# Kernel optimization log

Hardware: AMD Instinct MI355X
Metric: run time of the kernel (lower is better)

Reference implementation:

```python
import jax, jax.numpy as jnp
import numpy as np

U, I, D = 100000, 50000, 64
N = U + I
E_G, E_U, E_I = 2400000, 1600000, 800000


def _spmm(rows, cols, vals, x, n):
    # sparse [n, m] @ dense [m, d] via gather + scale + segment-sum scatter
    return jax.ops.segment_sum(x[cols] * vals[:, None], rows, num_segments=n)


def setup_inputs() -> dict:
    key = jax.random.key(0)
    ks = jax.random.split(key, 11)
    return {
        "user_emb": jax.random.normal(ks[0], (U, D), dtype=jnp.float32),
        "item_emb": jax.random.normal(ks[1], (I, D), dtype=jnp.float32),
        "graph_rows": jax.random.randint(ks[2], (E_G,), 0, N, dtype=jnp.int32),
        "graph_cols": jax.random.randint(ks[3], (E_G,), 0, N, dtype=jnp.int32),
        "graph_vals": jax.random.uniform(ks[4], (E_G,), dtype=jnp.float32),
        "user_rows": jax.random.randint(ks[5], (E_U,), 0, U, dtype=jnp.int32),
        "user_cols": jax.random.randint(ks[6], (E_U,), 0, U, dtype=jnp.int32),
        "user_vals": jax.random.uniform(ks[7], (E_U,), dtype=jnp.float32),
        "item_rows": jax.random.randint(ks[8], (E_I,), 0, I, dtype=jnp.int32),
        "item_cols": jax.random.randint(ks[9], (E_I,), 0, I, dtype=jnp.int32),
        "item_vals": jax.random.uniform(ks[10], (E_I,), dtype=jnp.float32),
    }


def reference(user_emb, item_emb,
              graph_rows, graph_cols, graph_vals,
              user_rows, user_cols, user_vals,
              item_rows, item_cols, item_vals):
    all_emb = jnp.concatenate([user_emb, item_emb], axis=0)  # [N, D]
    all_emb1 = _spmm(graph_rows, graph_cols, graph_vals, all_emb, N)
    user_emb2 = _spmm(user_rows, user_cols, user_vals, user_emb, U)
    item_emb2 = _spmm(item_rows, item_cols, item_vals, item_emb, I)
    user_emb1, item_emb1 = all_emb1[:U], all_emb1[U:]
    return (user_emb1, item_emb1, user_emb2, item_emb2)
```

## Files before the change

### kernel.cpp

```cpp
#include <hip/hip_runtime.h>

#define DDIM 64
constexpr int U_CNT = 100000;
constexpr int I_CNT = 50000;
constexpr int N_CNT = U_CNT + I_CNT;
constexpr int NB    = N_CNT + U_CNT + I_CNT;

constexpr int BIN_ROWS_LOG = 8;
constexpr int BIN_ROWS = 1 << BIN_ROWS_LOG;
constexpr int BINS = (NB + BIN_ROWS - 1) / BIN_ROWS;
constexpr int BINS_PAD = 1536;
constexpr int SORT_EDGES = 4096;
constexpr int HIST_EDGES = 32768;
constexpr int CAP = 4672;

constexpr int SB_LOG = 12;
constexpr int NSB = (NB + (1 << SB_LOG) - 1) >> SB_LOG;
constexpr int NSB_PAD = 128;

__device__ __forceinline__ int wave_incl_scan(int v, int lane) {
#pragma unroll
    for (int off = 1; off < 64; off <<= 1) {
        int t = __shfl_up(v, off, 64);
        if (lane >= off) v += t;
    }
    return v;
}

__device__ __forceinline__ unsigned short f2bf_rne(float f) {
    unsigned u = __float_as_uint(f);
    unsigned r = (u + 0x7FFFu + ((u >> 16) & 1u)) >> 16;
    return (unsigned short)r;
}

__global__ __launch_bounds__(256) void convert_emb(const float* __restrict__ ue,
                                                   const float* __restrict__ ie,
                                                   unsigned short* __restrict__ emb16) {
    int g = blockIdx.x * 256 + threadIdx.x;
    constexpr int UG = U_CNT * (DDIM / 4);
    constexpr int TG = N_CNT * (DDIM / 4);
    if (g >= TG) return;
    float4 v = (g < UG) ? ((const float4*)ue)[g] : ((const float4*)ie)[g - UG];
    ushort4 o;
    o.x = f2bf_rne(v.x); o.y = f2bf_rne(v.y); o.z = f2bf_rne(v.z); o.w = f2bf_rne(v.w);
    ((ushort4*)emb16)[g] = o;
}

__global__ __launch_bounds__(1024) void hist_pre(const int* __restrict__ gr,
                                                 const int* __restrict__ ur,
                                                 const int* __restrict__ ir,
                                                 int EG, int EU, int EI,
                                                 int* __restrict__ cnt) {
    __shared__ int h[BINS_PAD];
    for (int i = threadIdx.x; i < BINS_PAD; i += 1024) h[i] = 0;
    __syncthreads();
    int base = blockIdx.x * HIST_EDGES;
    int Et = EG + EU + EI;
    for (int j = 0; j < HIST_EDGES / 1024; ++j) {
        int e = base + j * 1024 + threadIdx.x;
        if (e < Et) {
            int b;
            if (e < EG)           b = gr[e];
            else if (e < EG + EU) b = N_CNT + ur[e - EG];
            else                  b = N_CNT + U_CNT + ir[e - EG - EU];
            atomicAdd(&h[b >> BIN_ROWS_LOG], 1);
        }
    }
    __syncthreads();
    for (int i = threadIdx.x; i < BINS; i += 1024) {
        int v = h[i];
        if (v) atomicAdd(&cnt[i], v);
    }
}

__global__ __launch_bounds__(1024) void scan_bins(const int* __restrict__ cnt,
                                                  int* __restrict__ bin_base,
                                                  int* __restrict__ bin_cursor,
                                                  int* __restrict__ sb_base,
                                                  int* __restrict__ sb_cursor,
                                                  int E_total) {
    __shared__ int wsum[16], woff[16];
    int tid = threadIdx.x, lane = tid & 63, wid = tid >> 6;
    int i0 = 2 * tid, i1 = 2 * tid + 1;
    int c0 = (i0 < BINS) ? cnt[i0] : 0;
    int c1 = (i1 < BINS) ? cnt[i1] : 0;
    int v = c0 + c1;
    int incl = wave_incl_scan(v, lane);
    if (lane == 63) wsum[wid] = incl;
    __syncthreads();
    if (wid == 0 && lane < 16) {
        int s = wsum[lane], si = s;
#pragma unroll
        for (int off = 1; off < 16; off <<= 1) {
            int t = __shfl_up(si, off, 64);
            if (lane >= off) si += t;
        }
        woff[lane] = si - s;
    }
    __syncthreads();
    int e = incl - v + woff[wid];
    if (i0 < BINS) { bin_base[i0] = e;      bin_cursor[i0] = e; }
    if (i1 < BINS) { bin_base[i1] = e + c0; bin_cursor[i1] = e + c0; }
    if (tid == 0) bin_base[BINS] = E_total;
    if (sb_base) {
        __syncthreads();
        if (tid <= NSB) {
            int idx = tid << (SB_LOG - BIN_ROWS_LOG);
            int vv = (idx >= BINS) ? E_total : bin_base[idx];
            sb_base[tid] = vv;
            if (tid < NSB) sb_cursor[tid] = vv;
        }
    }
}

__global__ __launch_bounds__(512) void sbsort(const int* __restrict__ rows,
                                              const int* __restrict__ cols,
                                              const float* __restrict__ vals, int E,
                                              int bucket_base, int gidx_base,
                                              int* __restrict__ sb_cursor,
                                              uint2* __restrict__ poolA) {
    __shared__ uint2 sorted[SORT_EDGES];
    __shared__ unsigned char ssb[SORT_EDGES];
    __shared__ int hist[NSB_PAD];
    __shared__ int lscan[NSB_PAD];
    __shared__ int lcur[NSB_PAD];
    __shared__ int wsum2[2];

    int tid = threadIdx.x, lane = tid & 63, wid = tid >> 6;
    for (int i = tid; i < NSB_PAD; i += 512) { hist[i] = 0; lcur[i] = 0; }
    __syncthreads();

    int start = blockIdx.x * SORT_EDGES;
    int base_e = start + tid * 8;
    int myb[8]; unsigned mylo[8]; float myv[8];
#pragma unroll
    for (int j = 0; j < 8; j += 4) {
        int e = base_e + j;
        if (e + 3 < E) {
            int4   r4 = *(const int4*)(rows + e);
            int4   c4 = *(const int4*)(cols + e);
            float4 v4 = *(const float4*)(vals + e);
            int rr[4] = {r4.x, r4.y, r4.z, r4.w};
            int cc[4] = {c4.x, c4.y, c4.z, c4.w};
            float vv[4] = {v4.x, v4.y, v4.z, v4.w};
#pragma unroll
            for (int q = 0; q < 4; ++q) {
                int bucket = bucket_base + rr[q];
                int sb = bucket >> SB_LOG;
                myb[j + q] = sb;
                mylo[j + q] = ((unsigned)(bucket & 4095) << 18) |
                              (unsigned)(gidx_base + cc[q]);
                myv[j + q] = vv[q];
                atomicAdd(&hist[sb], 1);
            }
        } else {
#pragma unroll
            for (int q = 0; q < 4; ++q) {
                int ee = e + q;
                if (ee < E) {
                    int bucket = bucket_base + rows[ee];
                    int sb = bucket >> SB_LOG;
                    myb[j + q] = sb;
                    mylo[j + q] = ((unsigned)(bucket & 4095) << 18) |
                                  (unsigned)(gidx_base + cols[ee]);
                    myv[j + q] = vals[ee];
                    atomicAdd(&hist[sb], 1);
                } else myb[j + q] = -1;
            }
        }
    }
    __syncthreads();

    int v = 0, incl = 0;
    if (tid < NSB_PAD) {
        v = hist[tid];
        incl = wave_incl_scan(v, lane);
        if (lane == 63) wsum2[wid] = incl;
    }
    __syncthreads();
    if (tid < NSB_PAD) {
        int st = incl - v + (wid ? wsum2[0] : 0);
        lscan[tid] = st;
        if (tid < NSB && v) hist[tid] = atomicAdd(&sb_cursor[tid], v);
    }
    __syncthreads();

#pragma unroll
    for (int j = 0; j < 8; ++j) {
        if (myb[j] >= 0) {
            int p = lscan[myb[j]] + atomicAdd(&lcur[myb[j]], 1);
            sorted[p] = make_uint2(mylo[j], __float_as_uint(myv[j]));
            ssb[p] = (unsigned char)myb[j];
        }
    }
    __syncthreads();

    int cntE = min(SORT_EDGES, E - start);
    for (int pos = tid; pos < cntE; pos += 512) {
        int b = ssb[pos];
        poolA[hist[b] + (pos - lscan[b])] = sorted[pos];
    }
}

__global__ __launch_bounds__(512) void binsort2(const uint2* __restrict__ poolA,
                                                const int* __restrict__ sb_base, int Et,
                                                int* __restrict__ bin_cursor,
                                                uint2* __restrict__ poolB) {
    __shared__ uint2 sorted[SORT_EDGES];
    __shared__ unsigned short sbin[SORT_EDGES];
    __shared__ int hist[BINS_PAD];
    __shared__ int lscan[BINS_PAD];
    __shared__ int lcur[BINS_PAD];
    __shared__ int wsum[8], woff[8];
    __shared__ int ssbb[NSB + 1];

    int tid = threadIdx.x, lane = tid & 63, wid = tid >> 6;
    for (int i = tid; i < BINS_PAD; i += 512) { hist[i] = 0; lcur[i] = 0; }
    if (tid <= NSB) ssbb[tid] = sb_base[tid];
    __syncthreads();

    int start = blockIdx.x * SORT_EDGES;
    int base_e = start + tid * 8;
    int sb;
    {
        int lo2 = 0, hi2 = NSB - 1;
        while (lo2 < hi2) {
            int mid = (lo2 + hi2 + 1) >> 1;
            if (ssbb[mid] <= base_e) lo2 = mid; else hi2 = mid - 1;
        }
        sb = lo2;
    }

    int myb[8]; uint2 myp[8];
#pragma unroll
    for (int j = 0; j < 8; j += 2) {
        int e = base_e + j;
        uint2 p0, p1;
        bool v1 = (e + 1 < Et), v0 = (e < Et);
        if (v1) {
            uint4 q = *(const uint4*)(poolA + e);
            p0 = make_uint2(q.x, q.y); p1 = make_uint2(q.z, q.w);
        } else if (v0) {
            p0 = poolA[e];
        }
        if (v0) {
            while (sb < NSB - 1 && e >= ssbb[sb + 1]) ++sb;
            int b = (sb << (SB_LOG - BIN_ROWS_LOG)) + (int)(p0.x >> 26);
            myb[j] = b; myp[j] = p0;
            atomicAdd(&hist[b], 1);
        } else myb[j] = -1;
        if (v1) {
            int e1 = e + 1;
            while (sb < NSB - 1 && e1 >= ssbb[sb + 1]) ++sb;
            int b = (sb << (SB_LOG - BIN_ROWS_LOG)) + (int)(p1.x >> 26);
            myb[j + 1] = b; myp[j + 1] = p1;
            atomicAdd(&hist[b], 1);
        } else myb[j + 1] = -1;
    }
    __syncthreads();

    int s0 = 3 * tid, s1 = s0 + 1, s2 = s0 + 2;
    int h0 = hist[s0], h1 = hist[s1], h2 = hist[s2];
    int v = h0 + h1 + h2;
    int incl = wave_incl_scan(v, lane);
    if (lane == 63) wsum[wid] = incl;
    __syncthreads();
    if (wid == 0 && lane < 8) {
        int s = wsum[lane], si = s;
#pragma unroll
        for (int off = 1; off < 8; off <<= 1) {
            int t = __shfl_up(si, off, 64);
            if (lane >= off) si += t;
        }
        woff[lane] = si - s;
    }
    __syncthreads();
    int e0 = incl - v + woff[wid];
    lscan[s0] = e0; lscan[s1] = e0 + h0; lscan[s2] = e0 + h0 + h1;
    if (s0 < BINS && h0) hist[s0] = atomicAdd(&bin_cursor[s0], h0);
    if (s1 < BINS && h1) hist[s1] = atomicAdd(&bin_cursor[s1], h1);
    if (s2 < BINS && h2) hist[s2] = atomicAdd(&bin_cursor[s2], h2);
    __syncthreads();

#pragma unroll
    for (int j = 0; j < 8; ++j) {
        if (myb[j] >= 0) {
            int p = lscan[myb[j]] + atomicAdd(&lcur[myb[j]], 1);
            sorted[p] = myp[j];
            sbin[p] = (unsigned short)myb[j];
        }
    }
    __syncthreads();

    int cntE = min(SORT_EDGES, Et - start);
    for (int pos = tid; pos < cntE; pos += 512) {
        int b = sbin[pos];
        poolB[hist[b] + (pos - lscan[b])] = sorted[pos];
    }
}

__global__ __launch_bounds__(512) void binsort(const int* __restrict__ rows,
                                               const int* __restrict__ cols,
                                               const float* __restrict__ vals, int E,
                                               int bucket_base, int gidx_base,
                                               int* __restrict__ bin_cursor,
                                               uint2* __restrict__ pool) {
    __shared__ uint2 sorted[SORT_EDGES];
    __shared__ unsigned short sbin[SORT_EDGES];
    __shared__ int hist[BINS_PAD];
    __shared__ int lscan[BINS_PAD];
    __shared__ int lcur[BINS_PAD];
    __shared__ int wsum[8], woff[8];

    int tid = threadIdx.x, lane = tid & 63, wid = tid >> 6;
    for (int i = tid; i < BINS_PAD; i += 512) { hist[i] = 0; lcur[i] = 0; }
    __syncthreads();

    int start = blockIdx.x * SORT_EDGES;
    int base_e = start + tid * 8;
    int myb[8]; unsigned mylo[8]; float myv[8];
#pragma unroll
    for (int j = 0; j < 8; j += 4) {
        int e = base_e + j;
        if (e + 3 < E) {
            int4   r4 = *(const int4*)(rows + e);
            int4   c4 = *(const int4*)(cols + e);
            float4 v4 = *(const float4*)(vals + e);
            int rr[4] = {r4.x, r4.y, r4.z, r4.w};
            int cc[4] = {c4.x, c4.y, c4.z, c4.w};
            float vv[4] = {v4.x, v4.y, v4.z, v4.w};
#pragma unroll
            for (int q = 0; q < 4; ++q) {
                int bucket = bucket_base + rr[q];
                myb[j + q] = bucket >> BIN_ROWS_LOG;
                mylo[j + q] = ((unsigned)(bucket & (BIN_ROWS - 1)) << 18) |
                              (unsigned)(gidx_base + cc[q]);
                myv[j + q] = vv[q];
                atomicAdd(&hist[myb[j + q]], 1);
            }
        } else {
#pragma unroll
            for (int q = 0; q < 4; ++q) {
                int ee = e + q;
                if (ee < E) {
                    int bucket = bucket_base + rows[ee];
                    myb[j + q] = bucket >> BIN_ROWS_LOG;
                    mylo[j + q] = ((unsigned)(bucket & (BIN_ROWS - 1)) << 18) |
                                  (unsigned)(gidx_base + cols[ee]);
                    myv[j + q] = vals[ee];
                    atomicAdd(&hist[myb[j + q]], 1);
                } else myb[j + q] = -1;
            }
        }
    }
    __syncthreads();

    int s0 = 3 * tid, s1 = s0 + 1, s2 = s0 + 2;
    int h0 = hist[s0], h1 = hist[s1], h2 = hist[s2];
    int v = h0 + h1 + h2;
    int incl = wave_incl_scan(v, lane);
    if (lane == 63) wsum[wid] = incl;
    __syncthreads();
    if (wid == 0 && lane < 8) {
        int s = wsum[lane], si = s;
#pragma unroll
        for (int off = 1; off < 8; off <<= 1) {
            int t = __shfl_up(si, off, 64);
            if (lane >= off) si += t;
        }
        woff[lane] = si - s;
    }
    __syncthreads();
    int e0 = incl - v + woff[wid];
    lscan[s0] = e0; lscan[s1] = e0 + h0; lscan[s2] = e0 + h0 + h1;
    if (s0 < BINS && h0) hist[s0] = atomicAdd(&bin_cursor[s0], h0);
    if (s1 < BINS && h1) hist[s1] = atomicAdd(&bin_cursor[s1], h1);
    if (s2 < BINS && h2) hist[s2] = atomicAdd(&bin_cursor[s2], h2);
    __syncthreads();

#pragma unroll
    for (int j = 0; j < 8; ++j) {
        if (myb[j] >= 0) {
            int p = lscan[myb[j]] + atomicAdd(&lcur[myb[j]], 1);
            sorted[p] = make_uint2(mylo[j], __float_as_uint(myv[j]));
            sbin[p] = (unsigned short)myb[j];
        }
    }
    __syncthreads();

    int cntE = min(SORT_EDGES, E - start);
    for (int pos = tid; pos < cntE; pos += 512) {
        int b = sbin[pos];
        pool[hist[b] + (pos - lscan[b])] = sorted[pos];
    }
}

template <bool BF16>
__global__ __launch_bounds__(512, 8) void refine_accum(const int* __restrict__ bin_base,
                                                       const uint2* __restrict__ pool,
                                                       const unsigned short* __restrict__ emb16,
                                                       const float* __restrict__ ue,
                                                       const float* __restrict__ ie,
                                                       float* __restrict__ out) {
    __shared__ uint2 sorted[CAP];
    __shared__ int rhist[BIN_ROWS];
    __shared__ int rstart[BIN_ROWS];
    __shared__ int rcur[BIN_ROWS];
    __shared__ int wsum[4];
    int tid = threadIdx.x, lane = tid & 63, wid = tid >> 6;
    int b = blockIdx.x;
    int s = bin_base[b], e = bin_base[b + 1];
    int cnt = min(e - s, CAP);

    if (tid < BIN_ROWS) rhist[tid] = 0;
    __syncthreads();

    const unsigned* px = (const unsigned*)pool;
    for (int i = tid; i < cnt; i += 512)
        atomicAdd(&rhist[(px[2 * (size_t)(s + i)] >> 18) & 255u], 1);
    __syncthreads();

    int v = 0, incl = 0;
    if (tid < BIN_ROWS) {
        v = rhist[tid];
        incl = wave_incl_scan(v, lane);
        if (lane == 63) wsum[wid] = incl;
    }
    __syncthreads();
    if (tid < BIN_ROWS) {
        int off = 0;
#pragma unroll
        for (int w = 0; w < 4; ++w)
            if (w < wid) off += wsum[w];
        int st = incl - v + off;
        rstart[tid] = st; rcur[tid] = st;
    }
    __syncthreads();

    for (int i = tid; i < cnt; i += 512) {
        uint2 p = pool[s + i];
        int pos = atomicAdd(&rcur[(p.x >> 18) & 255u], 1);
        sorted[pos] = p;
    }
    __syncthreads();

    long long rowbase = (long long)b * BIN_ROWS;
    auto gather = [&](unsigned gi) -> float {
        if (BF16) return __uint_as_float((unsigned)emb16[(gi << 6) + lane] << 16);
        return (gi < (unsigned)U_CNT) ? ue[((size_t)gi << 6) + lane]
                                      : ie[(((size_t)gi - U_CNT) << 6) + lane];
    };
    for (int r = wid; r < BIN_ROWS; r += 8) {
        long long row = rowbase + r;
        if (row >= NB) break;
        int k = rstart[r], ke = k + rhist[r];
        float acc0 = 0.f, acc1 = 0.f;
        for (; k + 8 <= ke; k += 8) {
            uint2 p0 = sorted[k],     p1 = sorted[k + 1], p2 = sorted[k + 2], p3 = sorted[k + 3];
            uint2 p4 = sorted[k + 4], p5 = sorted[k + 5], p6 = sorted[k + 6], p7 = sorted[k + 7];
            float x0 = gather(p0.x & 0x3FFFFu);
            float x1 = gather(p1.x & 0x3FFFFu);
            float x2 = gather(p2.x & 0x3FFFFu);
            float x3 = gather(p3.x & 0x3FFFFu);
            float x4 = gather(p4.x & 0x3FFFFu);
            float x5 = gather(p5.x & 0x3FFFFu);
            float x6 = gather(p6.x & 0x3FFFFu);
            float x7 = gather(p7.x & 0x3FFFFu);
            acc0 += __uint_as_float(p0.y) * x0;
            acc1 += __uint_as_float(p1.y) * x1;
            acc0 += __uint_as_float(p2.y) * x2;
            acc1 += __uint_as_float(p3.y) * x3;
            acc0 += __uint_as_float(p4.y) * x4;
            acc1 += __uint_as_float(p5.y) * x5;
            acc0 += __uint_as_float(p6.y) * x6;
            acc1 += __uint_as_float(p7.y) * x7;
        }
        for (; k + 4 <= ke; k += 4) {
            uint2 p0 = sorted[k], p1 = sorted[k + 1], p2 = sorted[k + 2], p3 = sorted[k + 3];
            float x0 = gather(p0.x & 0x3FFFFu);
            float x1 = gather(p1.x & 0x3FFFFu);
            float x2 = gather(p2.x & 0x3FFFFu);
            float x3 = gather(p3.x & 0x3FFFFu);
            acc0 += __uint_as_float(p0.y) * x0;
            acc1 += __uint_as_float(p1.y) * x1;
            acc0 += __uint_as_float(p2.y) * x2;
            acc1 += __uint_as_float(p3.y) * x3;
        }
        for (; k < ke; ++k) {
            uint2 p = sorted[k];
            acc0 += __uint_as_float(p.y) * gather(p.x & 0x3FFFFu);
        }
        out[(size_t)row * DDIM + lane] = acc0 + acc1;
    }
}

__global__ void spmm_graph_kernel(const int* __restrict__ rows, const int* __restrict__ cols,
                                  const float* __restrict__ vals,
                                  const float* __restrict__ user_emb,
                                  const float* __restrict__ item_emb,
                                  float* __restrict__ out, int E) {
    long long idx = (long long)blockIdx.x * blockDim.x + threadIdx.x;
    int e = (int)(idx >> 6), d = (int)(idx & 63);
    if (e >= E) return;
    int r = rows[e], c = cols[e];
    float v = vals[e];
    float x = (c < U_CNT) ? user_emb[(long long)c * DDIM + d]
                          : item_emb[(long long)(c - U_CNT) * DDIM + d];
    atomicAdd(&out[(long long)r * DDIM + d], v * x);
}

__global__ void spmm_plain_kernel(const int* __restrict__ rows, const int* __restrict__ cols,
                                  const float* __restrict__ vals,
                                  const float* __restrict__ emb,
                                  float* __restrict__ out, int E) {
    long long idx = (long long)blockIdx.x * blockDim.x + threadIdx.x;
    int e = (int)(idx >> 6), d = (int)(idx & 63);
    if (e >= E) return;
    int r = rows[e], c = cols[e];
    atomicAdd(&out[(long long)r * DDIM + d], vals[e] * emb[(long long)c * DDIM + d]);
}

extern "C" void kernel_launch(void* const* d_in, const int* in_sizes, int n_in,
                              void* d_out, int out_size, void* d_ws, size_t ws_size,
                              hipStream_t stream) {
    const float* user_emb = (const float*)d_in[0];
    const float* item_emb = (const float*)d_in[1];
    const int*   g_rows   = (const int*)d_in[2];
    const int*   g_cols   = (const int*)d_in[3];
    const float* g_vals   = (const float*)d_in[4];
    const int*   u_rows   = (const int*)d_in[5];
    const int*   u_cols   = (const int*)d_in[6];
    const float* u_vals   = (const float*)d_in[7];
    const int*   i_rows   = (const int*)d_in[8];
    const int*   i_cols   = (const int*)d_in[9];
    const float* i_vals   = (const float*)d_in[10];
    float* out = (float*)d_out;

    const int EG = in_sizes[2];
    const int EU = in_sizes[5];
    const int EI = in_sizes[8];
    const int Et = EG + EU + EI;

    const size_t emb_bytes = (size_t)N_CNT * DDIM * sizeof(unsigned short);

    size_t t_off_bb   = (size_t)BINS_PAD * sizeof(int);
    size_t t_off_bc   = t_off_bb + (size_t)(BINS + 1) * sizeof(int);
    size_t t_off_sbb  = t_off_bc + (size_t)BINS * sizeof(int);
    size_t t_off_sbc  = t_off_sbb + (size_t)(NSB + 1) * sizeof(int);
    size_t t_off_pa   = (t_off_sbc + (size_t)NSB * sizeof(int) + 15) & ~(size_t)15;
    size_t t_off_pb   = t_off_pa + (size_t)Et * sizeof(uint2);
    size_t needed_2p  = t_off_pb + (size_t)Et * sizeof(uint2);
    bool pa_fits_emb  = (size_t)Et * sizeof(uint2) >= emb_bytes;

    size_t o_off_base   = (size_t)BINS_PAD * sizeof(int);
    size_t o_off_cursor = o_off_base + (size_t)(BINS + 1) * sizeof(int);
    size_t o_off_pool   = (o_off_cursor + (size_t)BINS * sizeof(int) + 15) & ~(size_t)15;
    size_t o_off_emb    = o_off_pool + (size_t)Et * sizeof(uint2);
    size_t needed_min   = o_off_emb;
    size_t needed_full  = o_off_emb + emb_bytes;

    if (ws_size >= needed_2p && pa_fits_emb) {
        int*   cnt        = (int*)d_ws;
        int*   bin_base   = (int*)((char*)d_ws + t_off_bb);
        int*   bin_cursor = (int*)((char*)d_ws + t_off_bc);
        int*   sb_base    = (int*)((char*)d_ws + t_off_sbb);
        int*   sb_cursor  = (int*)((char*)d_ws + t_off_sbc);
        uint2* poolA      = (uint2*)((char*)d_ws + t_off_pa);
        uint2* poolB      = (uint2*)((char*)d_ws + t_off_pb);
        unsigned short* emb16 = (unsigned short*)poolA;

        hipMemsetAsync(cnt, 0, (size_t)BINS_PAD * sizeof(int), stream);

        unsigned hblocks = (unsigned)((Et + HIST_EDGES - 1) / HIST_EDGES);
        hist_pre<<<hblocks, 1024, 0, stream>>>(g_rows, u_rows, i_rows, EG, EU, EI, cnt);
        scan_bins<<<1, 1024, 0, stream>>>(cnt, bin_base, bin_cursor, sb_base, sb_cursor, Et);

        unsigned gb = (unsigned)((EG + SORT_EDGES - 1) / SORT_EDGES);
        unsigned ub = (unsigned)((EU + SORT_EDGES - 1) / SORT_EDGES);
        unsigned ib = (unsigned)((EI + SORT_EDGES - 1) / SORT_EDGES);
        sbsort<<<gb, 512, 0, stream>>>(g_rows, g_cols, g_vals, EG, 0,             0,     sb_cursor, poolA);
        sbsort<<<ub, 512, 0, stream>>>(u_rows, u_cols, u_vals, EU, N_CNT,         0,     sb_cursor, poolA);
        sbsort<<<ib, 512, 0, stream>>>(i_rows, i_cols, i_vals, EI, N_CNT + U_CNT, U_CNT, sb_cursor, poolA);

        unsigned b2 = (unsigned)((Et + SORT_EDGES - 1) / SORT_EDGES);
        binsort2<<<b2, 512, 0, stream>>>(poolA, sb_base, Et, bin_cursor, poolB);

        unsigned cgrid = (unsigned)((N_CNT * (DDIM / 4) + 255) / 256);
        convert_emb<<<cgrid, 256, 0, stream>>>(user_emb, item_emb, emb16);

        refine_accum<true><<<BINS, 512, 0, stream>>>(bin_base, poolB, emb16,
                                                     user_emb, item_emb, out);
    } else if (ws_size >= needed_min) {
        int*   cnt        = (int*)d_ws;
        int*   bin_base   = (int*)((char*)d_ws + o_off_base);
        int*   bin_cursor = (int*)((char*)d_ws + o_off_cursor);
        uint2* pool       = (uint2*)((char*)d_ws + o_off_pool);
        unsigned short* emb16 = (unsigned short*)((char*)d_ws + o_off_emb);
        bool use_bf16 = (ws_size >= needed_full);

        hipMemsetAsync(cnt, 0, (size_t)BINS_PAD * sizeof(int), stream);

        if (use_bf16) {
            unsigned cgrid = (unsigned)((N_CNT * (DDIM / 4) + 255) / 256);
            convert_emb<<<cgrid, 256, 0, stream>>>(user_emb, item_emb, emb16);
        }

        unsigned hblocks = (unsigned)((Et + HIST_EDGES - 1) / HIST_EDGES);
        hist_pre<<<hblocks, 1024, 0, stream>>>(g_rows, u_rows, i_rows, EG, EU, EI, cnt);
        scan_bins<<<1, 1024, 0, stream>>>(cnt, bin_base, bin_cursor, nullptr, nullptr, Et);

        unsigned gb = (unsigned)((EG + SORT_EDGES - 1) / SORT_EDGES);
        unsigned ub = (unsigned)((EU + SORT_EDGES - 1) / SORT_EDGES);
        unsigned ib = (unsigned)((EI + SORT_EDGES - 1) / SORT_EDGES);
        binsort<<<gb, 512, 0, stream>>>(g_rows, g_cols, g_vals, EG, 0,             0,     bin_cursor, pool);
        binsort<<<ub, 512, 0, stream>>>(u_rows, u_cols, u_vals, EU, N_CNT,         0,     bin_cursor, pool);
        binsort<<<ib, 512, 0, stream>>>(i_rows, i_cols, i_vals, EI, N_CNT + U_CNT, U_CNT, bin_cursor, pool);

        if (use_bf16)
            refine_accum<true><<<BINS, 512, 0, stream>>>(bin_base, pool, emb16,
                                                         user_emb, item_emb, out);
        else
            refine_accum<false><<<BINS, 512, 0, stream>>>(bin_base, pool, (const unsigned short*)nullptr,
                                                          user_emb, item_emb, out);
    } else {
        hipMemsetAsync(d_out, 0, (size_t)out_size * sizeof(float), stream);
        const int block = 256;
        {
            long long t = (long long)EG * DDIM;
            spmm_graph_kernel<<<(unsigned)((t + block - 1) / block), block, 0, stream>>>(
                g_rows, g_cols, g_vals, user_emb, item_emb, out, EG);
        }
        {
            long long t = (long long)EU * DDIM;
            spmm_plain_kernel<<<(unsigned)((t + block - 1) / block), block, 0, stream>>>(
                u_rows, u_cols, u_vals, user_emb, out + (size_t)N_CNT * DDIM, EU);
        }
        {
            long long t = (long long)EI * DDIM;
            spmm_plain_kernel<<<(unsigned)((t + block - 1) / block), block, 0, stream>>>(
                i_rows, i_cols, i_vals, item_emb, out + (size_t)(N_CNT + U_CNT) * DDIM, EI);
        }
    }
}
```

Baseline: 376.5 us.

## Fuse bf16 conversion into histogram, merge sort launches, window binsort2, nontemporal traffic

The bf16 embedding conversion now runs inside the histogram kernel, using a separate workspace region when it fits. The three per-matrix superbucket sort launches become one kernel. binsort2 keeps a 48-bin local window and scatters edges outside it directly with global atomics, replacing a 1536-entry shared scan. Loads and stores of the sort pools and output become nontemporal, and refine_accum caches its pool entries in registers so it no longer reads them twice. The aim is fewer launches and less memory traffic, at the cost of extra global atomics for out-of-window edges and a larger workspace requirement.

```diff
diff --git a/kernel.cpp b/kernel.cpp
--- a/kernel.cpp
+++ b/kernel.cpp
@@ -11,12 +11,17 @@
 constexpr int BINS = (NB + BIN_ROWS - 1) / BIN_ROWS;
 constexpr int BINS_PAD = 1536;
 constexpr int SORT_EDGES = 4096;
-constexpr int HIST_EDGES = 32768;
+constexpr int HIST_EDGES = 16384;
 constexpr int CAP = 4672;
+constexpr int NSLOT = 10;
 
 constexpr int SB_LOG = 12;
 constexpr int NSB = (NB + (1 << SB_LOG) - 1) >> SB_LOG;
 constexpr int NSB_PAD = 128;
+constexpr int BWIN = 48;
+
+typedef unsigned u32x2 __attribute__((ext_vector_type(2)));
+typedef unsigned u32x4 __attribute__((ext_vector_type(4)));
 
 __device__ __forceinline__ int wave_incl_scan(int v, int lane) {
 #pragma unroll
@@ -46,14 +51,30 @@
     ((ushort4*)emb16)[g] = o;
 }
 
-__global__ __launch_bounds__(1024) void hist_pre(const int* __restrict__ gr,
-                                                 const int* __restrict__ ur,
-                                                 const int* __restrict__ ir,
-                                                 int EG, int EU, int EI,
-                                                 int* __restrict__ cnt) {
+__global__ __launch_bounds__(1024) void hist_conv(const int* __restrict__ gr,
+                                                  const int* __restrict__ ur,
+                                                  const int* __restrict__ ir,
+                                                  int EG, int EU, int EI,
+                                                  int* __restrict__ cnt,
+                                                  const float* __restrict__ ue,
+                                                  const float* __restrict__ ie,
+                                                  unsigned short* __restrict__ emb16) {
     __shared__ int h[BINS_PAD];
     for (int i = threadIdx.x; i < BINS_PAD; i += 1024) h[i] = 0;
-    __syncthreads();
+
+    if (emb16) {
+        constexpr int UG = U_CNT * (DDIM / 4);
+        constexpr int TG = N_CNT * (DDIM / 4);
+        int stride = (int)gridDim.x * 1024;
+        for (int g = blockIdx.x * 1024 + threadIdx.x; g < TG; g += stride) {
+            float4 v = (g < UG) ? ((const float4*)ue)[g] : ((const float4*)ie)[g - UG];
+            ushort4 o;
+            o.x = f2bf_rne(v.x); o.y = f2bf_rne(v.y); o.z = f2bf_rne(v.z); o.w = f2bf_rne(v.w);
+            ((ushort4*)emb16)[g] = o;
+        }
+    }
+    __syncthreads();
+
     int base = blockIdx.x * HIST_EDGES;
     int Et = EG + EU + EI;
     for (int j = 0; j < HIST_EDGES / 1024; ++j) {
@@ -113,12 +134,12 @@
     }
 }
 
-__global__ __launch_bounds__(512) void sbsort(const int* __restrict__ rows,
-                                              const int* __restrict__ cols,
-                                              const float* __restrict__ vals, int E,
-                                              int bucket_base, int gidx_base,
-                                              int* __restrict__ sb_cursor,
-                                              uint2* __restrict__ poolA) {
+__global__ __launch_bounds__(512, 6) void sbsort_all(
+        const int* __restrict__ gr, const int* __restrict__ gc, const float* __restrict__ gv,
+        const int* __restrict__ ur, const int* __restrict__ uc, const float* __restrict__ uv,
+        const int* __restrict__ ir, const int* __restrict__ ic, const float* __restrict__ iv,
+        int EG, int EU, int EI,
+        int* __restrict__ sb_cursor, uint2* __restrict__ poolA) {
     __shared__ uint2 sorted[SORT_EDGES];
     __shared__ unsigned char ssb[SORT_EDGES];
     __shared__ int hist[NSB_PAD];
@@ -130,26 +151,33 @@
     for (int i = tid; i < NSB_PAD; i += 512) { hist[i] = 0; lcur[i] = 0; }
     __syncthreads();
 
+    const int Et = EG + EU + EI;
     int start = blockIdx.x * SORT_EDGES;
     int base_e = start + tid * 8;
     int myb[8]; unsigned mylo[8]; float myv[8];
+
 #pragma unroll
     for (int j = 0; j < 8; j += 4) {
         int e = base_e + j;
-        if (e + 3 < E) {
-            int4   r4 = *(const int4*)(rows + e);
-            int4   c4 = *(const int4*)(cols + e);
-            float4 v4 = *(const float4*)(vals + e);
+        int sg0 = (e < EG) ? 0 : (e < EG + EU ? 1 : 2);
+        int sg3 = (e + 3 < EG) ? 0 : (e + 3 < EG + EU ? 1 : 2);
+        if (e + 3 < Et && sg0 == sg3) {
+            const int* R; const int* Cc; const float* V; int boff, goff, loc;
+            if (sg0 == 0)      { R = gr; Cc = gc; V = gv; boff = 0;             goff = 0;     loc = e; }
+            else if (sg0 == 1) { R = ur; Cc = uc; V = uv; boff = N_CNT;         goff = 0;     loc = e - EG; }
+            else               { R = ir; Cc = ic; V = iv; boff = N_CNT + U_CNT; goff = U_CNT; loc = e - EG - EU; }
+            int4   r4 = *(const int4*)(R + loc);
+            int4   c4 = *(const int4*)(Cc + loc);
+            float4 v4 = *(const float4*)(V + loc);
             int rr[4] = {r4.x, r4.y, r4.z, r4.w};
             int cc[4] = {c4.x, c4.y, c4.z, c4.w};
             float vv[4] = {v4.x, v4.y, v4.z, v4.w};
 #pragma unroll
             for (int q = 0; q < 4; ++q) {
-                int bucket = bucket_base + rr[q];
+                int bucket = boff + rr[q];
                 int sb = bucket >> SB_LOG;
                 myb[j + q] = sb;
-                mylo[j + q] = ((unsigned)(bucket & 4095) << 18) |
-                              (unsigned)(gidx_base + cc[q]);
+                mylo[j + q] = ((unsigned)(bucket & 4095) << 18) | (unsigned)(goff + cc[q]);
                 myv[j + q] = vv[q];
                 atomicAdd(&hist[sb], 1);
             }
@@ -157,13 +185,16 @@
 #pragma unroll
             for (int q = 0; q < 4; ++q) {
                 int ee = e + q;
-                if (ee < E) {
-                    int bucket = bucket_base + rows[ee];
+                if (ee < Et) {
+                    int r, c; float vl; int boff, goff;
+                    if (ee < EG)           { r = gr[ee]; c = gc[ee]; vl = gv[ee]; boff = 0; goff = 0; }
+                    else if (ee < EG + EU) { int k = ee - EG;      r = ur[k]; c = uc[k]; vl = uv[k]; boff = N_CNT;         goff = 0; }
+                    else                   { int k = ee - EG - EU; r = ir[k]; c = ic[k]; vl = iv[k]; boff = N_CNT + U_CNT; goff = U_CNT; }
+                    int bucket = boff + r;
                     int sb = bucket >> SB_LOG;
                     myb[j + q] = sb;
-                    mylo[j + q] = ((unsigned)(bucket & 4095) << 18) |
-                                  (unsigned)(gidx_base + cols[ee]);
-                    myv[j + q] = vals[ee];
+                    mylo[j + q] = ((unsigned)(bucket & 4095) << 18) | (unsigned)(goff + c);
+                    myv[j + q] = vl;
                     atomicAdd(&hist[sb], 1);
                 } else myb[j + q] = -1;
             }
@@ -195,27 +226,29 @@
     }
     __syncthreads();
 
-    int cntE = min(SORT_EDGES, E - start);
+    int cntE = min(SORT_EDGES, Et - start);
     for (int pos = tid; pos < cntE; pos += 512) {
         int b = ssb[pos];
-        poolA[hist[b] + (pos - lscan[b])] = sorted[pos];
-    }
-}
-
-__global__ __launch_bounds__(512) void binsort2(const uint2* __restrict__ poolA,
-                                                const int* __restrict__ sb_base, int Et,
-                                                int* __restrict__ bin_cursor,
-                                                uint2* __restrict__ poolB) {
+        uint2 t = sorted[pos];
+        u32x2 q; q.x = t.x; q.y = t.y;
+        __builtin_nontemporal_store(q, (u32x2*)&poolA[hist[b] + (pos - lscan[b])]);
+    }
+}
+
+__global__ __launch_bounds__(512, 6) void binsort2(const uint2* __restrict__ poolA,
+                                                   const int* __restrict__ sb_base, int Et,
+                                                   int* __restrict__ bin_cursor,
+                                                   uint2* __restrict__ poolB) {
     __shared__ uint2 sorted[SORT_EDGES];
-    __shared__ unsigned short sbin[SORT_EDGES];
-    __shared__ int hist[BINS_PAD];
-    __shared__ int lscan[BINS_PAD];
-    __shared__ int lcur[BINS_PAD];
-    __shared__ int wsum[8], woff[8];
+    __shared__ unsigned char sbin[SORT_EDGES];
+    __shared__ int hist[BWIN];
+    __shared__ int lscan[BWIN];
+    __shared__ int lcur[BWIN];
     __shared__ int ssbb[NSB + 1];
-
-    int tid = threadIdx.x, lane = tid & 63, wid = tid >> 6;
-    for (int i = tid; i < BINS_PAD; i += 512) { hist[i] = 0; lcur[i] = 0; }
+    __shared__ int W0s, nloc;
+
+    int tid = threadIdx.x, lane = tid & 63;
+    if (tid < BWIN) { hist[tid] = 0; }
     if (tid <= NSB) ssbb[tid] = sb_base[tid];
     __syncthreads();
 
@@ -230,6 +263,9 @@
         }
         sb = lo2;
     }
+    if (tid == 0) W0s = sb << (SB_LOG - BIN_ROWS_LOG);
+    __syncthreads();
+    int W0 = W0s;
 
     int myb[8]; uint2 myp[8];
 #pragma unroll
@@ -238,64 +274,69 @@
         uint2 p0, p1;
         bool v1 = (e + 1 < Et), v0 = (e < Et);
         if (v1) {
-            uint4 q = *(const uint4*)(poolA + e);
-            p0 = make_uint2(q.x, q.y); p1 = make_uint2(q.z, q.w);
+            u32x4 q = __builtin_nontemporal_load((const u32x4*)(poolA + e));
+            p0.x = q.x; p0.y = q.y; p1.x = q.z; p1.y = q.w;
         } else if (v0) {
-            p0 = poolA[e];
+            u32x2 q = __builtin_nontemporal_load((const u32x2*)(poolA + e));
+            p0.x = q.x; p0.y = q.y;
         }
         if (v0) {
             while (sb < NSB - 1 && e >= ssbb[sb + 1]) ++sb;
             int b = (sb << (SB_LOG - BIN_ROWS_LOG)) + (int)(p0.x >> 26);
-            myb[j] = b; myp[j] = p0;
-            atomicAdd(&hist[b], 1);
+            int slot = b - W0;
+            if ((unsigned)slot < (unsigned)BWIN) {
+                myb[j] = slot; myp[j] = p0;
+                atomicAdd(&hist[slot], 1);
+            } else {
+                int gp = atomicAdd(&bin_cursor[b], 1);
+                poolB[gp] = p0;
+                myb[j] = -1;
+            }
         } else myb[j] = -1;
         if (v1) {
             int e1 = e + 1;
             while (sb < NSB - 1 && e1 >= ssbb[sb + 1]) ++sb;
             int b = (sb << (SB_LOG - BIN_ROWS_LOG)) + (int)(p1.x >> 26);
-            myb[j + 1] = b; myp[j + 1] = p1;
-            atomicAdd(&hist[b], 1);
+            int slot = b - W0;
+            if ((unsigned)slot < (unsigned)BWIN) {
+                myb[j + 1] = slot; myp[j + 1] = p1;
+                atomicAdd(&hist[slot], 1);
+            } else {
+                int gp = atomicAdd(&bin_cursor[b], 1);
+                poolB[gp] = p1;
+                myb[j + 1] = -1;
+            }
         } else myb[j + 1] = -1;
     }
     __syncthreads();
 
-    int s0 = 3 * tid, s1 = s0 + 1, s2 = s0 + 2;
-    int h0 = hist[s0], h1 = hist[s1], h2 = hist[s2];
-    int v = h0 + h1 + h2;
-    int incl = wave_incl_scan(v, lane);
-    if (lane == 63) wsum[wid] = incl;
-    __syncthreads();
-    if (wid == 0 && lane < 8) {
-        int s = wsum[lane], si = s;
-#pragma unroll
-        for (int off = 1; off < 8; off <<= 1) {
-            int t = __shfl_up(si, off, 64);
-            if (lane >= off) si += t;
-        }
-        woff[lane] = si - s;
-    }
-    __syncthreads();
-    int e0 = incl - v + woff[wid];
-    lscan[s0] = e0; lscan[s1] = e0 + h0; lscan[s2] = e0 + h0 + h1;
-    if (s0 < BINS && h0) hist[s0] = atomicAdd(&bin_cursor[s0], h0);
-    if (s1 < BINS && h1) hist[s1] = atomicAdd(&bin_cursor[s1], h1);
-    if (s2 < BINS && h2) hist[s2] = atomicAdd(&bin_cursor[s2], h2);
+    if (tid < 64) {
+        int vv = (tid < BWIN) ? hist[tid] : 0;
+        int incl = wave_incl_scan(vv, lane);
+        if (tid < BWIN) { lscan[tid] = incl - vv; lcur[tid] = incl - vv; }
+        if (tid == BWIN - 1) nloc = incl;
+    }
+    __syncthreads();
+    if (tid < BWIN && hist[tid] > 0)
+        hist[tid] = atomicAdd(&bin_cursor[W0 + tid], hist[tid]);
     __syncthreads();
 
 #pragma unroll
     for (int j = 0; j < 8; ++j) {
         if (myb[j] >= 0) {
-            int p = lscan[myb[j]] + atomicAdd(&lcur[myb[j]], 1);
+            int p = atomicAdd(&lcur[myb[j]], 1);
             sorted[p] = myp[j];
-            sbin[p] = (unsigned short)myb[j];
-        }
-    }
-    __syncthreads();
-
-    int cntE = min(SORT_EDGES, Et - start);
-    for (int pos = tid; pos < cntE; pos += 512) {
-        int b = sbin[pos];
-        poolB[hist[b] + (pos - lscan[b])] = sorted[pos];
+            sbin[p] = (unsigned char)myb[j];
+        }
+    }
+    __syncthreads();
+
+    int tot = nloc;
+    for (int pos = tid; pos < tot; pos += 512) {
+        int sl = sbin[pos];
+        uint2 t = sorted[pos];
+        u32x2 q; q.x = t.x; q.y = t.y;
+        __builtin_nontemporal_store(q, (u32x2*)&poolB[hist[sl] + (pos - lscan[sl])]);
     }
 }
 
@@ -415,9 +456,17 @@
     if (tid < BIN_ROWS) rhist[tid] = 0;
     __syncthreads();
 
-    const unsigned* px = (const unsigned*)pool;
-    for (int i = tid; i < cnt; i += 512)
-        atomicAdd(&rhist[(px[2 * (size_t)(s + i)] >> 18) & 255u], 1);
+    uint2 my[NSLOT];
+    const u32x2* poolv = (const u32x2*)(pool + s);
+#pragma unroll
+    for (int j = 0; j < NSLOT; ++j) {
+        int idx = tid + j * 512;
+        if (idx < cnt) {
+            u32x2 q = __builtin_nontemporal_load(poolv + idx);
+            my[j].x = q.x; my[j].y = q.y;
+            atomicAdd(&rhist[(q.x >> 18) & 255u], 1);
+        }
+    }
     __syncthreads();
 
     int v = 0, incl = 0;
@@ -437,10 +486,13 @@
     }
     __syncthreads();
 
-    for (int i = tid; i < cnt; i += 512) {
-        uint2 p = pool[s + i];
-        int pos = atomicAdd(&rcur[(p.x >> 18) & 255u], 1);
-        sorted[pos] = p;
+#pragma unroll
+    for (int j = 0; j < NSLOT; ++j) {
+        int idx = tid + j * 512;
+        if (idx < cnt) {
+            int pos = atomicAdd(&rcur[(my[j].x >> 18) & 255u], 1);
+            sorted[pos] = my[j];
+        }
     }
     __syncthreads();
 
@@ -490,7 +542,7 @@
             uint2 p = sorted[k];
             acc0 += __uint_as_float(p.y) * gather(p.x & 0x3FFFFu);
         }
-        out[(size_t)row * DDIM + lane] = acc0 + acc1;
+        __builtin_nontemporal_store(acc0 + acc1, &out[(size_t)row * DDIM + lane]);
     }
 }
 
@@ -550,6 +602,8 @@
     size_t t_off_pa   = (t_off_sbc + (size_t)NSB * sizeof(int) + 15) & ~(size_t)15;
     size_t t_off_pb   = t_off_pa + (size_t)Et * sizeof(uint2);
     size_t needed_2p  = t_off_pb + (size_t)Et * sizeof(uint2);
+    size_t t_off_emb  = (needed_2p + 15) & ~(size_t)15;
+    size_t needed_na  = t_off_emb + emb_bytes;
     bool pa_fits_emb  = (size_t)Et * sizeof(uint2) >= emb_bytes;
 
     size_t o_off_base   = (size_t)BINS_PAD * sizeof(int);
@@ -560,6 +614,7 @@
     size_t needed_full  = o_off_emb + emb_bytes;
 
     if (ws_size >= needed_2p && pa_fits_emb) {
+        bool noalias = (ws_size >= needed_na);
         int*   cnt        = (int*)d_ws;
         int*   bin_base   = (int*)((char*)d_ws + t_off_bb);
         int*   bin_cursor = (int*)((char*)d_ws + t_off_bc);
@@ -567,26 +622,28 @@
         int*   sb_cursor  = (int*)((char*)d_ws + t_off_sbc);
         uint2* poolA      = (uint2*)((char*)d_ws + t_off_pa);
         uint2* poolB      = (uint2*)((char*)d_ws + t_off_pb);
-        unsigned short* emb16 = (unsigned short*)poolA;
+        unsigned short* emb16 = noalias ? (unsigned short*)((char*)d_ws + t_off_emb)
+                                        : (unsigned short*)poolA;
 
         hipMemsetAsync(cnt, 0, (size_t)BINS_PAD * sizeof(int), stream);
 
         unsigned hblocks = (unsigned)((Et + HIST_EDGES - 1) / HIST_EDGES);
-        hist_pre<<<hblocks, 1024, 0, stream>>>(g_rows, u_rows, i_rows, EG, EU, EI, cnt);
+        hist_conv<<<hblocks, 1024, 0, stream>>>(g_rows, u_rows, i_rows, EG, EU, EI, cnt,
+                                                user_emb, item_emb,
+                                                noalias ? emb16 : (unsigned short*)nullptr);
         scan_bins<<<1, 1024, 0, stream>>>(cnt, bin_base, bin_cursor, sb_base, sb_cursor, Et);
 
-        unsigned gb = (unsigned)((EG + SORT_EDGES - 1) / SORT_EDGES);
-        unsigned ub = (unsigned)((EU + SORT_EDGES - 1) / SORT_EDGES);
-        unsigned ib = (unsigned)((EI + SORT_EDGES - 1) / SORT_EDGES);
-        sbsort<<<gb, 512, 0, stream>>>(g_rows, g_cols, g_vals, EG, 0,             0,     sb_cursor, poolA);
-        sbsort<<<ub, 512, 0, stream>>>(u_rows, u_cols, u_vals, EU, N_CNT,         0,     sb_cursor, poolA);
-        sbsort<<<ib, 512, 0, stream>>>(i_rows, i_cols, i_vals, EI, N_CNT + U_CNT, U_CNT, sb_cursor, poolA);
-
-        unsigned b2 = (unsigned)((Et + SORT_EDGES - 1) / SORT_EDGES);
-        binsort2<<<b2, 512, 0, stream>>>(poolA, sb_base, Et, bin_cursor, poolB);
-
-        unsigned cgrid = (unsigned)((N_CNT * (DDIM / 4) + 255) / 256);
-        convert_emb<<<cgrid, 256, 0, stream>>>(user_emb, item_emb, emb16);
+        unsigned nb2 = (unsigned)((Et + SORT_EDGES - 1) / SORT_EDGES);
+        sbsort_all<<<nb2, 512, 0, stream>>>(g_rows, g_cols, g_vals,
+                                            u_rows, u_cols, u_vals,
+                                            i_rows, i_cols, i_vals,
+                                            EG, EU, EI, sb_cursor, poolA);
+        binsort2<<<nb2, 512, 0, stream>>>(poolA, sb_base, Et, bin_cursor, poolB);
+
+        if (!noalias) {
+            unsigned cgrid = (unsigned)((N_CNT * (DDIM / 4) + 255) / 256);
+            convert_emb<<<cgrid, 256, 0, stream>>>(user_emb, item_emb, emb16);
+        }
 
         refine_accum<true><<<BINS, 512, 0, stream>>>(bin_base, poolB, emb16,
                                                      user_emb, item_emb, out);
@@ -600,13 +657,10 @@
 
         hipMemsetAsync(cnt, 0, (size_t)BINS_PAD * sizeof(int), stream);
 
-        if (use_bf16) {
-            unsigned cgrid = (unsigned)((N_CNT * (DDIM / 4) + 255) / 256);
-            convert_emb<<<cgrid, 256, 0, stream>>>(user_emb, item_emb, emb16);
-        }
-
         unsigned hblocks = (unsigned)((Et + HIST_EDGES - 1) / HIST_EDGES);
-        hist_pre<<<hblocks, 1024, 0, stream>>>(g_rows, u_rows, i_rows, EG, EU, EI, cnt);
+        hist_conv<<<hblocks, 1024, 0, stream>>>(g_rows, u_rows, i_rows, EG, EU, EI, cnt,
+                                                user_emb, item_emb,
+                                                use_bf16 ? emb16 : (unsigned short*)nullptr);
         scan_bins<<<1, 1024, 0, stream>>>(cnt, bin_base, bin_cursor, nullptr, nullptr, Et);
 
         unsigned gb = (unsigned)((EG + SORT_EDGES - 1) / SORT_EDGES);
```

Result: faster. 357.0 us (-5.2%).
